# Performance work log

Measured on AMD Instinct MI355X. Metric: run time of the kernel, lower is better.

## Reference

```python
import jax, jax.numpy as jnp
import numpy as np
from jax import lax

B, T, U, V = 4, 200, 100, 1024
D_ENC, D_DEC, J = 144, 320, 320


def setup_inputs() -> dict:
    key = jax.random.key(0)
    ks = jax.random.split(key, 8)
    s = lambda d: 1.0 / np.sqrt(d).astype(np.float32)
    return {
        "enc_out": jax.random.normal(ks[0], (B, T, D_ENC), jnp.float32),
        "dec_out": jax.random.normal(ks[1], (B, U + 1, D_DEC), jnp.float32),
        "W_enc": jax.random.normal(ks[2], (D_ENC, J), jnp.float32) * s(D_ENC),
        "b_enc": jnp.zeros((J,), jnp.float32),
        "W_dec": jax.random.normal(ks[3], (D_DEC, J), jnp.float32) * s(D_DEC),
        "b_dec": jnp.zeros((J,), jnp.float32),
        "W_out": jax.random.normal(ks[4], (J, V), jnp.float32) * s(J),
        "b_out": jnp.zeros((V,), jnp.float32),
        "targets": jax.random.randint(ks[5], (B, U), 1, V, jnp.int32),
        "enc_lengths": jax.random.randint(ks[6], (B,), T // 2, T + 1, jnp.int32),
        "target_lengths": jax.random.randint(ks[7], (B,), U // 2, U + 1, jnp.int32),
    }


def _rnnt_loss(log_probs, targets, enc_lengths, target_lengths):
    # log_probs: [B, T, U+1, V]; blank index = 0 (matches RNNTLoss(blank=0))
    blank_lp = log_probs[..., 0]  # [B, T, U+1]
    idx = jnp.broadcast_to(targets[:, None, :, None].astype(jnp.int32), (B, T, U, 1))
    emit_lp = jnp.take_along_axis(log_probs[:, :, :U, :], idx, axis=-1)[..., 0]  # [B, T, U]

    # alpha[0, u] = sum of emit log-probs along u at t=0
    alpha0 = jnp.concatenate(
        [jnp.zeros((B, 1), log_probs.dtype), jnp.cumsum(emit_lp[:, 0, :], axis=1)], axis=1
    )  # [B, U+1]

    def row(a, emit_t):
        # a: alpha_prev + blank (vertical transitions), [B, U+1]; emit_t: [B, U]
        def step(prev, xs):
            a_u, e_prev = xs
            cur = jnp.logaddexp(a_u, prev + e_prev)
            return cur, cur
        _, rest = lax.scan(step, a[:, 0], (a[:, 1:].T, emit_t.T))  # rest: [U, B]
        return jnp.concatenate([a[:, :1], rest.T], axis=1)

    def t_step(alpha_prev, xs):
        blank_prev, emit_t = xs
        alpha_t = row(alpha_prev + blank_prev, emit_t)
        return alpha_t, alpha_t

    xs = (jnp.swapaxes(blank_lp[:, :-1, :], 0, 1), jnp.swapaxes(emit_lp[:, 1:, :], 0, 1))
    _, alphas_rest = lax.scan(t_step, alpha0, xs)  # [T-1, B, U+1]
    alphas = jnp.concatenate([alpha0[None], alphas_rest], axis=0)  # [T, B, U+1]

    b_idx = jnp.arange(B)
    t_idx = enc_lengths - 1
    ll = alphas[t_idx, b_idx, target_lengths] + blank_lp[b_idx, t_idx, target_lengths]
    return jnp.mean(-ll)  # reduction='mean' over batch


def reference(enc_out, dec_out, W_enc, b_enc, W_dec, b_dec, W_out, b_out, targets, enc_lengths, target_lengths):
    enc_p = enc_out @ W_enc + b_enc  # [B, T, J]
    dec_p = dec_out @ W_dec + b_dec  # [B, U+1, J]
    joint = jnp.tanh(enc_p[:, :, None, :] + dec_p[:, None, :, :])  # [B, T, U+1, J]
    logits = joint @ W_out + b_out  # [B, T, U+1, V]
    log_probs = jax.nn.log_softmax(logits, axis=-1)
    return _rnnt_loss(log_probs, targets, enc_lengths, target_lengths)
```

## Files before the change

### kernel.cpp

```cpp
#include <hip/hip_runtime.h>
#include <hip/hip_bf16.h>
#include <math.h>

#define B_ 4
#define T_ 200
#define U_ 100
#define V_ 1024
#define DE 144
#define DD 320
#define J_ 320
#define M_TOT (B_ * T_ * (U_ + 1))
#define SSTR 328
#define DSTR 104
#define NDIAG 300
#define LOG2E 1.4426950408889634f
#define LN2 0.6931471805599453f

typedef __attribute__((ext_vector_type(8))) short bf16x8_t;
typedef __attribute__((ext_vector_type(4))) float f32x4_t;

__device__ __forceinline__ float fast_tanh(float x) {
    float e = __builtin_amdgcn_exp2f(x * (2.0f * LOG2E));
    float r = __builtin_amdgcn_rcpf(e + 1.0f);
    return fmaf(-2.0f, r, 1.0f);
}

__device__ __forceinline__ ushort f2bf(float x) {
    uint u = __float_as_uint(x);
    uint r = (u + 0x7FFFu + ((u >> 16) & 1u)) >> 16;
    return (ushort)r;
}

template <int K>
__device__ __forceinline__ void proj_body(const float* __restrict__ X,
                                          const float* __restrict__ W,
                                          const float* __restrict__ bias,
                                          float* __restrict__ Y,
                                          int r0, int R, float* sx, int tid) {
    constexpr int QK = K / 4;
    for (int q = tid; q < 16 * QK; q += 640) {
        int row = q / QK;
        int kq = q - row * QK;
        int r = r0 + row;
        if (r >= R) r = R - 1;
        *(float4*)&sx[row * K + kq * 4] = *(const float4*)&X[r * K + kq * 4];
    }
    __syncthreads();
    const int half = (tid >= 320) ? 1 : 0;
    const int c = tid - half * 320;
    float acc[8];
#pragma unroll
    for (int i = 0; i < 8; i++) acc[i] = 0.0f;
    for (int k = 0; k < K; k += 4) {
        float w0 = W[(k + 0) * 320 + c];
        float w1 = W[(k + 1) * 320 + c];
        float w2 = W[(k + 2) * 320 + c];
        float w3 = W[(k + 3) * 320 + c];
#pragma unroll
        for (int i = 0; i < 8; i++) {
            const float4 x4 = *(const float4*)&sx[(half * 8 + i) * K + k];
            acc[i] = fmaf(x4.x, w0, acc[i]);
            acc[i] = fmaf(x4.y, w1, acc[i]);
            acc[i] = fmaf(x4.z, w2, acc[i]);
            acc[i] = fmaf(x4.w, w3, acc[i]);
        }
    }
    const float bb = bias[c];
#pragma unroll
    for (int i = 0; i < 8; i++) {
        int r = r0 + half * 8 + i;
        if (r < R) Y[r * 320 + c] = acc[i] + bb;
    }
}

__global__ __launch_bounds__(640) void prep_kernel(
    const float* __restrict__ enc_out, const float* __restrict__ dec_out,
    const float* __restrict__ W_enc, const float* __restrict__ b_enc,
    const float* __restrict__ W_dec, const float* __restrict__ b_dec,
    const float* __restrict__ W_out,
    float* __restrict__ enc_p, float* __restrict__ dec_p,
    ushort* __restrict__ Wt) {
    __shared__ float sx[16 * 320];
    const int bid = blockIdx.x;
    const int tid = threadIdx.x;
    if (bid < 50) {
        proj_body<DE>(enc_out, W_enc, b_enc, enc_p, bid * 16, B_ * T_, sx, tid);
    } else if (bid < 76) {
        proj_body<DD>(dec_out, W_dec, b_dec, dec_p, (bid - 50) * 16,
                      B_ * (U_ + 1), sx, tid);
    } else {
        int o8 = (bid - 76) * 640 + tid;
        int frag = o8 >> 6;
        int lane8 = o8 & 63;
        int fv = frag / 10;
        int fk = frag - fv * 10;
        int v = fv * 16 + (lane8 & 15);
        int kbase = fk * 32 + ((lane8 >> 4) << 3);
        ushort tmp[8];
#pragma unroll
        for (int e = 0; e < 8; e++) tmp[e] = f2bf(W_out[(kbase + e) * 1024 + v]);
        *(ushort4*)&Wt[o8 * 8] = *(ushort4*)&tmp[0];
        *(ushort4*)&Wt[o8 * 8 + 4] = *(ushort4*)&tmp[4];
    }
}

__global__ __launch_bounds__(1024, 4) void joint_mfma(
    const float* __restrict__ enc_p, const float* __restrict__ dec_p,
    const ushort* __restrict__ Wt, const float* __restrict__ b_out,
    const int* __restrict__ targets,
    float* __restrict__ bsk, float* __restrict__ esk) {
    __shared__ ushort sh[64 * SSTR];
    __shared__ float parts[16][64];
    __shared__ float lse_sh[64];
    __shared__ int tgt_sh[64];
    __shared__ int skb_sh[64];

    const int tid = threadIdx.x;
    const int r0 = blockIdx.x * 64;

    if (tid < 64) {
        int rc = r0 + tid;
        int tg = -1, skb = -1;
        if (rc < M_TOT) {
            int b = rc / 20200;
            int rem = rc - b * 20200;
            int t = rem / 101;
            int u = rem - t * 101;
            skb = (b * NDIAG + t + u) * DSTR + u;
            if (u < U_) tg = targets[b * U_ + u];
        }
        tgt_sh[tid] = tg;
        skb_sh[tid] = skb;
    }

    {
        const int si = tid >> 4;
        const int sq = tid & 15;
        int rc = r0 + si;
        if (rc > M_TOT - 1) rc = M_TOT - 1;
        int b = rc / 20200;
        int rem = rc - b * 20200;
        int t = rem / 101;
        int u = rem - t * 101;
        const float4* ep = (const float4*)&enc_p[(b * 200 + t) * 320];
        const float4* dp = (const float4*)&dec_p[(b * 101 + u) * 320];
        ushort* shp = &sh[si * SSTR];
#pragma unroll
        for (int it = 0; it < 5; it++) {
            int kq = sq + it * 16;
            float4 e = ep[kq];
            float4 dd = dp[kq];
            float t0 = fast_tanh(e.x + dd.x);
            float t1 = fast_tanh(e.y + dd.y);
            float t2 = fast_tanh(e.z + dd.z);
            float t3 = fast_tanh(e.w + dd.w);
            __hip_bfloat162 p0 = __float22bfloat162_rn(make_float2(t0, t1));
            __hip_bfloat162 p1 = __float22bfloat162_rn(make_float2(t2, t3));
            uint2 pk;
            pk.x = *(uint*)&p0;
            pk.y = *(uint*)&p1;
            *(uint2*)&shp[kq * 4] = pk;
        }
    }
    __syncthreads();

    const int wave = tid >> 6;
    const int lane = tid & 63;
    const int lrow = lane & 15;
    const int lk = (lane >> 4) * 8;
    const int cb16 = wave * 4;

    f32x4_t acc[4][4];
#pragma unroll
    for (int mt = 0; mt < 4; mt++)
#pragma unroll
        for (int nt = 0; nt < 4; nt++) acc[mt][nt] = (f32x4_t)(0.0f);

    for (int ks = 0; ks < 10; ks++) {
        bf16x8_t a[4];
#pragma unroll
        for (int mt = 0; mt < 4; mt++)
            a[mt] = *(const bf16x8_t*)&sh[(mt * 16 + lrow) * SSTR + ks * 32 + lk];
#pragma unroll
        for (int nt = 0; nt < 4; nt++) {
            bf16x8_t bfr = *(const bf16x8_t*)&Wt[(((cb16 + nt) * 10 + ks) << 9) + lane * 8];
#pragma unroll
            for (int mt = 0; mt < 4; mt++)
                acc[mt][nt] = __builtin_amdgcn_mfma_f32_16x16x32_bf16(a[mt], bfr, acc[mt][nt], 0, 0, 0);
        }
    }

    float boL[4];
#pragma unroll
    for (int nt = 0; nt < 4; nt++)
        boL[nt] = b_out[wave * 64 + nt * 16 + lrow] * LOG2E;

#pragma unroll
    for (int mt = 0; mt < 4; mt++) {
#pragma unroll
        for (int j = 0; j < 4; j++) {
            float s = __builtin_amdgcn_exp2f(fmaf(acc[mt][0][j], LOG2E, boL[0]));
            s += __builtin_amdgcn_exp2f(fmaf(acc[mt][1][j], LOG2E, boL[1]));
            s += __builtin_amdgcn_exp2f(fmaf(acc[mt][2][j], LOG2E, boL[2]));
            s += __builtin_amdgcn_exp2f(fmaf(acc[mt][3][j], LOG2E, boL[3]));
#pragma unroll
            for (int off = 1; off < 16; off <<= 1)
                s += __shfl_xor(s, off, 16);
            if (lrow == 0) {
                int row = mt * 16 + (lane >> 4) * 4 + j;
                parts[wave][row] = s;
            }
        }
    }
    __syncthreads();
    if (tid < 64) {
        float s = parts[0][tid];
#pragma unroll
        for (int w = 1; w < 16; w++) s += parts[w][tid];
        lse_sh[tid] = __builtin_amdgcn_logf(s) * LN2;
    }
    __syncthreads();

#pragma unroll
    for (int mt = 0; mt < 4; mt++) {
#pragma unroll
        for (int j = 0; j < 4; j++) {
            int lr = mt * 16 + (lane >> 4) * 4 + j;
            int skb = skb_sh[lr];
            if (skb < 0) continue;
            int tc = tgt_sh[lr];
            bool isblank = (wave == 0) && (lrow == 0);
            bool isemit = (tc >= 0) && ((tc >> 6) == wave) && ((tc & 15) == lrow);
            if (isblank || isemit) {
                float lse = lse_sh[lr];
                if (isblank)
                    bsk[skb] = fmaf(boL[0], LN2, acc[mt][0][j]) - lse;
                if (isemit) {
                    int ntl = (tc >> 4) & 3;
                    float v = fmaf(boL[0], LN2, acc[mt][0][j]);
#pragma unroll
                    for (int nt = 1; nt < 4; nt++)
                        if (nt == ntl) v = fmaf(boL[nt], LN2, acc[mt][nt][j]);
                    esk[skb] = v - lse;
                }
            }
        }
    }
}

__global__ __launch_bounds__(256, 1) void alpha_c2_kernel(
    const float* __restrict__ bsk, const float* __restrict__ esk,
    const int* __restrict__ enc_len, const int* __restrict__ tgt_len,
    float* __restrict__ out) {
    __shared__ float ll_sh[B_];
    const int tid = threadIdx.x;
    const int b = tid >> 6;
    const int l = tid & 63;
    const float* Bp = bsk + b * (NDIAG * DSTR);
    const float* Ep = esk + b * (NDIAG * DSTR);
    const int el = enc_len[b];
    const int tl = tgt_len[b];
    const int dfin = el - 1 + tl;

    const int u0 = 2 * l;
    const bool ok0 = (u0 <= U_);
    const bool ok1 = (u0 + 1 <= U_);
    const int uc = ok0 ? u0 : 0;

    float A0 = (l == 0) ? 0.0f : -INFINITY;
    float A1 = -INFINITY;

    float2 rb[16], re[16];
#pragma unroll
    for (int k = 0; k < 16; k++) {
        rb[k] = *(const float2*)&Bp[k * DSTR + uc];
        re[k] = *(const float2*)&Ep[k * DSTR + uc];
    }

    for (int dc = 1; dc <= 289; dc += 16) {
#pragma unroll
        for (int q = 0; q < 16; q++) {
            const int d = dc + q;
            if (d > NDIAG - 1) continue;
            const int sc = q;
            const int sm = (q + 1) & 15;
            float2 cb = rb[sc], ce = re[sc];
            float2 mb = rb[sm];
            int dn = d + 15;
            if (dn > NDIAG - 1) dn = NDIAG - 1;
            rb[sc] = *(const float2*)&Bp[dn * DSTR + uc];
            re[sc] = *(const float2*)&Ep[dn * DSTR + uc];

            float s = A1 + ce.y;
            float sn = __shfl_up(s, 1, 64);

            float va0 = A0 + cb.x;
            float vb0 = (l >= 1) ? sn : -INFINITY;
            float va1 = A1 + cb.y;
            float vb1 = A0 + ce.x;

            float M0 = fmaxf(va0, vb0);
            float n0 = (M0 == -INFINITY)
                           ? -INFINITY
                           : M0 + __logf(1.0f + __expf(fminf(va0, vb0) - M0));
            float M1 = fmaxf(va1, vb1);
            float n1 = (M1 == -INFINITY)
                           ? -INFINITY
                           : M1 + __logf(1.0f + __expf(fminf(va1, vb1) - M1));

            const int t0 = d - u0;
            if (!ok0 || t0 < 0 || t0 >= T_) n0 = -INFINITY;
            if (!ok1 || (t0 - 1) < 0 || (t0 - 1) >= T_) n1 = -INFINITY;

            if (d == dfin) {
                if (tl == u0) ll_sh[b] = n0 + mb.x;
                if (tl == u0 + 1) ll_sh[b] = n1 + mb.y;
            }
            A0 = n0;
            A1 = n1;
        }
    }
    __syncthreads();
    if (tid == 0)
        out[0] = -0.25f * (ll_sh[0] + ll_sh[1] + ll_sh[2] + ll_sh[3]);
}

extern "C" void kernel_launch(void* const* d_in, const int* in_sizes, int n_in,
                              void* d_out, int out_size, void* d_ws, size_t ws_size,
                              hipStream_t stream) {
    const float* enc_out = (const float*)d_in[0];
    const float* dec_out = (const float*)d_in[1];
    const float* W_enc = (const float*)d_in[2];
    const float* b_enc = (const float*)d_in[3];
    const float* W_dec = (const float*)d_in[4];
    const float* b_dec = (const float*)d_in[5];
    const float* W_out = (const float*)d_in[6];
    const float* b_out = (const float*)d_in[7];
    const int* targets = (const int*)d_in[8];
    const int* enc_len = (const int*)d_in[9];
    const int* tgt_len = (const int*)d_in[10];

    float* ws = (float*)d_ws;
    float* enc_p = ws;
    float* dec_p = enc_p + B_ * T_ * J_;
    float* bsk = dec_p + B_ * (U_ + 1) * J_;
    float* esk = bsk + B_ * NDIAG * DSTR;
    ushort* Wt = (ushort*)(esk + B_ * NDIAG * DSTR);

    prep_kernel<<<140, 640, 0, stream>>>(enc_out, dec_out, W_enc, b_enc,
                                         W_dec, b_dec, W_out, enc_p, dec_p, Wt);

    joint_mfma<<<(M_TOT + 63) / 64, 1024, 0, stream>>>(
        enc_p, dec_p, Wt, b_out, targets, bsk, esk);

    alpha_c2_kernel<<<1, 256, 0, stream>>>(bsk, esk, enc_len, tgt_len,
                                           (float*)d_out);
}
```

Before: 191.8 us.

## Retile joint GEMM to 128 rows by half-vocab with LDS-staged double-buffered weights

The joint MFMA kernel now handles 128 rows per block and splits the vocabulary into two halves across paired blocks. Output-weight fragments are double-buffered into LDS with direct global-to-LDS loads instead of being read per wave from global memory. Because the softmax denominator now spans two blocks, partial exp-sums and raw blank/emit logits go to scratch buffers, and a new combine kernel computes the log-sum-exp and scatters into the diagonal layout. This trades an extra launch and extra memory traffic, plus a per-k-step barrier, for better weight reuse and more rows per block. Each tile's tanh activations are also recomputed in both vocabulary-half blocks.

```diff
diff --git a/kernel.cpp b/kernel.cpp
--- a/kernel.cpp
+++ b/kernel.cpp
@@ -10,6 +10,7 @@
 #define DD 320
 #define J_ 320
 #define M_TOT (B_ * T_ * (U_ + 1))
+#define M_PAD 80896
 #define SSTR 328
 #define DSTR 104
 #define NDIAG 300
@@ -29,6 +30,12 @@
     uint u = __float_as_uint(x);
     uint r = (u + 0x7FFFu + ((u >> 16) & 1u)) >> 16;
     return (ushort)r;
+}
+
+__device__ __forceinline__ void gload_lds16(const void* g, void* l) {
+    __builtin_amdgcn_global_load_lds(
+        (const __attribute__((address_space(1))) unsigned int*)g,
+        (__attribute__((address_space(3))) unsigned int*)l, 16, 0, 0);
 }
 
 template <int K>
@@ -108,34 +115,44 @@
     const float* __restrict__ enc_p, const float* __restrict__ dec_p,
     const ushort* __restrict__ Wt, const float* __restrict__ b_out,
     const int* __restrict__ targets,
-    float* __restrict__ bsk, float* __restrict__ esk) {
-    __shared__ ushort sh[64 * SSTR];
-    __shared__ float parts[16][64];
-    __shared__ float lse_sh[64];
-    __shared__ int tgt_sh[64];
-    __shared__ int skb_sh[64];
+    float* __restrict__ sarr, float* __restrict__ pbl,
+    float* __restrict__ pem) {
+    __shared__ ushort sh[128 * SSTR];
+    __shared__ ushort wt[2][16384];
+    __shared__ float parts[8][128];
+    __shared__ int tgt_sh[128];
 
     const int tid = threadIdx.x;
-    const int r0 = blockIdx.x * 64;
-
-    if (tid < 64) {
+    const int bid = blockIdx.x;
+    const int tile = bid >> 1;
+    const int hf = bid & 1;
+    const int r0 = tile * 128;
+    const int wave = tid >> 6;
+    const int lane = tid & 63;
+
+    {
+        const int f0 = wave * 2;
+        gload_lds16(&Wt[(((hf * 32 + f0) * 10 + 0) << 9) + lane * 8],
+                    &wt[0][f0 * 512]);
+        gload_lds16(&Wt[(((hf * 32 + f0 + 1) * 10 + 0) << 9) + lane * 8],
+                    &wt[0][(f0 + 1) * 512]);
+    }
+
+    if (tid < 128) {
         int rc = r0 + tid;
-        int tg = -1, skb = -1;
+        int tg = -1;
         if (rc < M_TOT) {
             int b = rc / 20200;
             int rem = rc - b * 20200;
-            int t = rem / 101;
-            int u = rem - t * 101;
-            skb = (b * NDIAG + t + u) * DSTR + u;
+            int u = rem - (rem / 101) * 101;
             if (u < U_) tg = targets[b * U_ + u];
         }
         tgt_sh[tid] = tg;
-        skb_sh[tid] = skb;
     }
 
     {
-        const int si = tid >> 4;
-        const int sq = tid & 15;
+        const int si = tid >> 3;
+        const int sq = tid & 7;
         int rc = r0 + si;
         if (rc > M_TOT - 1) rc = M_TOT - 1;
         int b = rc / 20200;
@@ -146,8 +163,8 @@
         const float4* dp = (const float4*)&dec_p[(b * 101 + u) * 320];
         ushort* shp = &sh[si * SSTR];
 #pragma unroll
-        for (int it = 0; it < 5; it++) {
-            int kq = sq + it * 16;
+        for (int it = 0; it < 10; it++) {
+            int kq = it * 8 + sq;
             float4 e = ep[kq];
             float4 dd = dp[kq];
             float t0 = fast_tanh(e.x + dd.x);
@@ -164,11 +181,10 @@
     }
     __syncthreads();
 
-    const int wave = tid >> 6;
-    const int lane = tid & 63;
     const int lrow = lane & 15;
     const int lk = (lane >> 4) * 8;
-    const int cb16 = wave * 4;
+    const int rg = wave >> 3;
+    const int cs = wave & 7;
 
     f32x4_t acc[4][4];
 #pragma unroll
@@ -176,24 +192,34 @@
 #pragma unroll
         for (int nt = 0; nt < 4; nt++) acc[mt][nt] = (f32x4_t)(0.0f);
 
+    int cur = 0;
     for (int ks = 0; ks < 10; ks++) {
+        if (ks < 9) {
+            const int f0 = wave * 2;
+            gload_lds16(&Wt[(((hf * 32 + f0) * 10 + ks + 1) << 9) + lane * 8],
+                        &wt[cur ^ 1][f0 * 512]);
+            gload_lds16(&Wt[(((hf * 32 + f0 + 1) * 10 + ks + 1) << 9) + lane * 8],
+                        &wt[cur ^ 1][(f0 + 1) * 512]);
+        }
         bf16x8_t a[4];
 #pragma unroll
         for (int mt = 0; mt < 4; mt++)
-            a[mt] = *(const bf16x8_t*)&sh[(mt * 16 + lrow) * SSTR + ks * 32 + lk];
+            a[mt] = *(const bf16x8_t*)&sh[(rg * 64 + mt * 16 + lrow) * SSTR + ks * 32 + lk];
 #pragma unroll
         for (int nt = 0; nt < 4; nt++) {
-            bf16x8_t bfr = *(const bf16x8_t*)&Wt[(((cb16 + nt) * 10 + ks) << 9) + lane * 8];
+            bf16x8_t bfr = *(const bf16x8_t*)&wt[cur][(cs * 4 + nt) * 512 + lane * 8];
 #pragma unroll
             for (int mt = 0; mt < 4; mt++)
                 acc[mt][nt] = __builtin_amdgcn_mfma_f32_16x16x32_bf16(a[mt], bfr, acc[mt][nt], 0, 0, 0);
         }
+        __syncthreads();
+        cur ^= 1;
     }
 
     float boL[4];
 #pragma unroll
     for (int nt = 0; nt < 4; nt++)
-        boL[nt] = b_out[wave * 64 + nt * 16 + lrow] * LOG2E;
+        boL[nt] = b_out[hf * 512 + cs * 64 + nt * 16 + lrow] * LOG2E;
 
 #pragma unroll
     for (int mt = 0; mt < 4; mt++) {
@@ -206,46 +232,57 @@
 #pragma unroll
             for (int off = 1; off < 16; off <<= 1)
                 s += __shfl_xor(s, off, 16);
-            if (lrow == 0) {
-                int row = mt * 16 + (lane >> 4) * 4 + j;
-                parts[wave][row] = s;
+            if (lrow == 0)
+                parts[cs][rg * 64 + mt * 16 + (lane >> 4) * 4 + j] = s;
+        }
+    }
+    __syncthreads();
+    if (tid < 128) {
+        float s = parts[0][tid];
+#pragma unroll
+        for (int w = 1; w < 8; w++) s += parts[w][tid];
+        int r = r0 + tid;
+        if (r < M_TOT) sarr[r * 2 + hf] = s;
+    }
+
+#pragma unroll
+    for (int mt = 0; mt < 4; mt++) {
+#pragma unroll
+        for (int j = 0; j < 4; j++) {
+            int lr = rg * 64 + mt * 16 + (lane >> 4) * 4 + j;
+            int r = r0 + lr;
+            if (r >= M_TOT) continue;
+            int tc = tgt_sh[lr];
+            bool isblank = (hf == 0) && (cs == 0) && (lrow == 0);
+            bool isemit = (tc >= 0) && ((tc >> 9) == hf) &&
+                          (((tc >> 6) & 7) == cs) && ((tc & 15) == lrow);
+            if (isblank) pbl[r] = fmaf(boL[0], LN2, acc[mt][0][j]);
+            if (isemit) {
+                int ntl = (tc >> 4) & 3;
+                float v = fmaf(boL[0], LN2, acc[mt][0][j]);
+#pragma unroll
+                for (int nt = 1; nt < 4; nt++)
+                    if (nt == ntl) v = fmaf(boL[nt], LN2, acc[mt][nt][j]);
+                pem[r] = v;
             }
         }
     }
-    __syncthreads();
-    if (tid < 64) {
-        float s = parts[0][tid];
-#pragma unroll
-        for (int w = 1; w < 16; w++) s += parts[w][tid];
-        lse_sh[tid] = __builtin_amdgcn_logf(s) * LN2;
-    }
-    __syncthreads();
-
-#pragma unroll
-    for (int mt = 0; mt < 4; mt++) {
-#pragma unroll
-        for (int j = 0; j < 4; j++) {
-            int lr = mt * 16 + (lane >> 4) * 4 + j;
-            int skb = skb_sh[lr];
-            if (skb < 0) continue;
-            int tc = tgt_sh[lr];
-            bool isblank = (wave == 0) && (lrow == 0);
-            bool isemit = (tc >= 0) && ((tc >> 6) == wave) && ((tc & 15) == lrow);
-            if (isblank || isemit) {
-                float lse = lse_sh[lr];
-                if (isblank)
-                    bsk[skb] = fmaf(boL[0], LN2, acc[mt][0][j]) - lse;
-                if (isemit) {
-                    int ntl = (tc >> 4) & 3;
-                    float v = fmaf(boL[0], LN2, acc[mt][0][j]);
-#pragma unroll
-                    for (int nt = 1; nt < 4; nt++)
-                        if (nt == ntl) v = fmaf(boL[nt], LN2, acc[mt][nt][j]);
-                    esk[skb] = v - lse;
-                }
-            }
-        }
-    }
+}
+
+__global__ __launch_bounds__(256) void combine_kernel(
+    const float* __restrict__ sarr, const float* __restrict__ pbl,
+    const float* __restrict__ pem,
+    float* __restrict__ bsk, float* __restrict__ esk) {
+    int r = blockIdx.x * 256 + threadIdx.x;
+    if (r >= M_TOT) return;
+    float lse = __builtin_amdgcn_logf(sarr[2 * r] + sarr[2 * r + 1]) * LN2;
+    int b = r / 20200;
+    int rem = r - b * 20200;
+    int t = rem / 101;
+    int u = rem - t * 101;
+    int skb = (b * NDIAG + t + u) * DSTR + u;
+    bsk[skb] = pbl[r] - lse;
+    if (u < U_) esk[skb] = pem[r] - lse;
 }
 
 __global__ __launch_bounds__(256, 1) void alpha_c2_kernel(
@@ -345,13 +382,19 @@
     float* dec_p = enc_p + B_ * T_ * J_;
     float* bsk = dec_p + B_ * (U_ + 1) * J_;
     float* esk = bsk + B_ * NDIAG * DSTR;
-    ushort* Wt = (ushort*)(esk + B_ * NDIAG * DSTR);
+    float* sarr = esk + B_ * NDIAG * DSTR;
+    float* pbl = sarr + 2 * M_PAD;
+    float* pem = pbl + M_PAD;
+    ushort* Wt = (ushort*)(pem + M_PAD);
 
     prep_kernel<<<140, 640, 0, stream>>>(enc_out, dec_out, W_enc, b_enc,
                                          W_dec, b_dec, W_out, enc_p, dec_p, Wt);
 
-    joint_mfma<<<(M_TOT + 63) / 64, 1024, 0, stream>>>(
-        enc_p, dec_p, Wt, b_out, targets, bsk, esk);
+    joint_mfma<<<(M_PAD / 128) * 2, 1024, 0, stream>>>(
+        enc_p, dec_p, Wt, b_out, targets, sarr, pbl, pem);
+
+    combine_kernel<<<(M_TOT + 255) / 256, 256, 0, stream>>>(sarr, pbl, pem,
+                                                            bsk, esk);
 
     alpha_c2_kernel<<<1, 256, 0, stream>>>(bsk, esk, enc_len, tgt_len,
                                            (float*)d_out);
```

Result: slower. 198.2 us (+3.3%).
